# Performance work log

Hardware: AMD Instinct MI355X
Metric: run time of the kernel (lower is better)

The kernel has to match this reference:

```python
import jax, jax.numpy as jnp
import numpy as np

N_HEADS = 8
HEAD_DIM = 32
KSIZE = 3
IN_CH = 128
OUT_CH = 256


def setup_inputs() -> dict:
    key = jax.random.key(0)
    k1, k2, k3, k4 = jax.random.split(key, 4)
    x = jax.random.normal(k1, (8, IN_CH, 64, 64), dtype=jnp.float32)
    w_key = jax.random.normal(k2, (N_HEADS * HEAD_DIM, IN_CH), dtype=jnp.float32) * 0.05
    b_key = jax.random.normal(k3, (N_HEADS * HEAD_DIM,), dtype=jnp.float32) * 0.05
    # memory init in torch: uniform in [-1, 1)
    memory = jax.random.uniform(k4, (N_HEADS, HEAD_DIM * KSIZE * KSIZE, OUT_CH // N_HEADS),
                                dtype=jnp.float32) * 2.0 - 1.0
    return {"x": x, "w_key": w_key, "b_key": b_key, "memory": memory}


def _unfold(z, k):
    # z: [b, C, Hp, Wp] padded; returns [b, C*k*k, H*W] with torch.unfold layout
    b, C, Hp, Wp = z.shape
    H, W = Hp - k + 1, Wp - k + 1
    patches = [z[:, :, i:i + H, j:j + W] for i in range(k) for j in range(k)]
    # stack -> [b, C, k*k, H, W]; channel-major like torch unfold (C outer, kh*k+kw inner)
    p = jnp.stack(patches, axis=2)
    return p.reshape(b, C * k * k, H * W)


def reference(x, w_key, b_key, memory):
    b, c_in, H, W = x.shape
    k = KSIZE
    m = N_HEADS
    # 1x1 conv (to_mem_key)
    key_map = jnp.einsum('oi,bihw->bohw', w_key, x) + b_key[None, :, None, None]
    # ZeroPad2d((k//2, k%2, k//2, k%2)) = (left, right, top, bottom)
    pl, pr = k // 2, k % 2
    padded = jnp.pad(key_map, ((0, 0), (0, 0), (pl, pr), (pl, pr)))
    unf = _unfold(padded, k)                      # [b, C*k*k, L], C = m*head_dim
    ckk = unf.shape[1]
    L = unf.shape[2]
    c = ckk // m
    # rearrange 'b (c m) l -> b m c l' (m is the FAST factor, per einops pattern)
    attn = unf.reshape(b, c, m, L).transpose(0, 2, 1, 3)   # [b, m, c, L]
    attn = jax.nn.softmax(attn, axis=2)
    out = jnp.einsum('nki,bnkl->bnil', memory, attn)       # [b, m, head_out, L]
    # rearrange 'b m c (h w) -> b (m c) h w'
    return out.reshape(b, m * out.shape[2], H, W)
```

## Files before the change

kernel.cpp:

```cpp
#include <hip/hip_runtime.h>

#define B_   8
#define CIN  128
#define CKEY 256
#define NH   8
#define HOUT 32
#define CPH  288
#define HW   4096

#define XSTR   136
#define ESTR   264
#define EROW   (66 * ESTR)
#define E2_BYTES   (3 * EROW * 2)
#define XBUF_BYTES (64 * XSTR * 2)
#define SMEM_BYTES (E2_BYTES + 2 * XBUF_BYTES)

typedef __attribute__((ext_vector_type(8))) short bf16x8;
typedef __attribute__((ext_vector_type(4))) float f32x4;

__device__ __forceinline__ unsigned short f2bf(float f) {
  unsigned u = __builtin_bit_cast(unsigned, f);
  u += 0x7FFFu + ((u >> 16) & 1u);
  return (unsigned short)(u >> 16);
}

__global__ __launch_bounds__(256) void wfragP_prep(
    const float* __restrict__ wk, unsigned short* __restrict__ wfragP)
{
  const int idx  = blockIdx.x * 256 + threadIdx.x;
  const int lane = idx & 63, fi = idx >> 6;
  const int ks = fi & 3, sh = (fi >> 2) & 1, cm = fi >> 3;
  const int li = lane & 15, q = lane >> 4;
  const int och = cm + 8 * (sh * 16 + li);
  const int ic0 = ks * 32 + q * 8;
  unsigned short* dst = wfragP + (size_t)idx * 8;
#pragma unroll
  for (int j = 0; j < 8; ++j) dst[j] = f2bf(wk[och * CIN + ic0 + j]);
}

__global__ __launch_bounds__(256) void mfragP_prep(
    const float* __restrict__ mem, unsigned short* __restrict__ mfragP)
{
  const int idx  = blockIdx.x * 256 + threadIdx.x;
  const int lane = idx & 63, fi = idx >> 6;
  const int ib = fi & 1, pm = fi >> 1;
  const int p = pm % 9, m = pm / 9;
  const int li = lane & 15, q = lane >> 4;
  const int i  = ib * 16 + li;
  unsigned short* dst = mfragP + (size_t)idx * 8;
#pragma unroll
  for (int j = 0; j < 8; ++j) {
    const int s = q * 8 + j;
    const int c = ((m - p + 8) & 7) + 8 * s;
    const int t = (9 * c + p) >> 3;
    dst[j] = f2bf(mem[(m * CPH + t) * HOUT + i]);
  }
}

__global__ __launch_bounds__(512, 2) void fused_kernel(
    const float* __restrict__ x, const unsigned short* __restrict__ wfragP,
    const unsigned short* __restrict__ mfragP, const float* __restrict__ bk,
    float* __restrict__ out)
{
  extern __shared__ char smem[];
  unsigned short* e2  = (unsigned short*)smem;
  unsigned short* xb0 = (unsigned short*)(smem + E2_BYTES);
  unsigned short* xb1 = xb0 + 64 * XSTR;
  float* tileb = (float*)(smem + E2_BYTES);

  const int tid = threadIdx.x;
  const int bid = blockIdx.x;
  const int b = bid & 7, h = bid >> 3;
  const int lane = tid & 63;
  const int wv = __builtin_amdgcn_readfirstlane(tid >> 6);
  const int li = lane & 15, q = lane >> 4;

  float bias[2][4];
#pragma unroll
  for (int sh = 0; sh < 2; ++sh)
#pragma unroll
    for (int r = 0; r < 4; ++r)
      bias[sh][r] = bk[wv + 8 * (sh * 16 + 4 * q + r)];

  const int spx = tid & 63, sicg = tid >> 6;
  const int sxor = ((spx >> 3) & 7) << 3;

  auto stage_load = [&](int y, unsigned* pk) {
    const float* xr = x + (size_t)b * CIN * HW + y * 64 + spx;
#pragma unroll
    for (int r4 = 0; r4 < 4; ++r4) {
      const int ic0 = 4 * sicg + 32 * r4;
      const float v0 = xr[(size_t)(ic0 + 0) * HW];
      const float v1 = xr[(size_t)(ic0 + 1) * HW];
      const float v2 = xr[(size_t)(ic0 + 2) * HW];
      const float v3 = xr[(size_t)(ic0 + 3) * HW];
      pk[2 * r4 + 0] = (unsigned)f2bf(v0) | ((unsigned)f2bf(v1) << 16);
      pk[2 * r4 + 1] = (unsigned)f2bf(v2) | ((unsigned)f2bf(v3) << 16);
    }
  };
  auto stage_write = [&](unsigned short* xb, const unsigned* pk) {
    unsigned* xdw = (unsigned*)xb;
#pragma unroll
    for (int r4 = 0; r4 < 4; ++r4) {
      const int o = (2 * sicg + 16 * r4) ^ sxor;
      *(uint2*)(xdw + spx * 68 + o) = make_uint2(pk[2 * r4], pk[2 * r4 + 1]);
    }
  };

  auto conv_row = [&](const unsigned short* xb, int rrow) {
    f32x4 acc[2][4];
#pragma unroll
    for (int sh = 0; sh < 2; ++sh)
#pragma unroll
      for (int pt = 0; pt < 4; ++pt) {
        f32x4 cv; cv[0] = bias[sh][0]; cv[1] = bias[sh][1];
        cv[2] = bias[sh][2]; cv[3] = bias[sh][3];
        acc[sh][pt] = cv;
      }
    const unsigned* xdw = (const unsigned*)xb;
#pragma unroll
    for (int ks = 0; ks < 4; ++ks) {
      const bf16x8 a0 = *(const bf16x8*)(
          wfragP + ((size_t)(((wv * 2 + 0) * 4 + ks) * 64 + lane)) * 8);
      const bf16x8 a1 = *(const bf16x8*)(
          wfragP + ((size_t)(((wv * 2 + 1) * 4 + ks) * 64 + lane)) * 8);
#pragma unroll
      for (int pt = 0; pt < 4; ++pt) {
        const int px  = pt * 16 + li;
        const int blk = (ks * 16 + q * 4) ^ (((px >> 3) & 7) << 3);
        const bf16x8 bfr = *(const bf16x8*)(xdw + px * 68 + blk);
        acc[0][pt] = __builtin_amdgcn_mfma_f32_16x16x32_bf16(a0, bfr, acc[0][pt], 0, 0, 0);
        acc[1][pt] = __builtin_amdgcn_mfma_f32_16x16x32_bf16(a1, bfr, acc[1][pt], 0, 0, 0);
      }
    }
    unsigned short* erow = e2 + rrow * EROW;
#pragma unroll
    for (int sh = 0; sh < 2; ++sh)
#pragma unroll
      for (int pt = 0; pt < 4; ++pt) {
        const float w0 = __expf(acc[sh][pt][0]);
        const float w1 = __expf(acc[sh][pt][1]);
        const float w2 = __expf(acc[sh][pt][2]);
        const float w3 = __expf(acc[sh][pt][3]);
        const unsigned d0 = (unsigned)f2bf(w0) | ((unsigned)f2bf(w1) << 16);
        const unsigned d1 = (unsigned)f2bf(w2) | ((unsigned)f2bf(w3) << 16);
        unsigned short* dst = erow + (pt * 16 + li + 1) * ESTR
                            + wv * 32 + sh * 16 + 4 * q;
        *(uint2*)dst = make_uint2(d0, d1);
      }
    if (tid < 256) {
      const int xcol = (tid & 1) ? 65 : 0;
      ((unsigned*)(erow + xcol * ESTR))[tid >> 1] = 0x3F803F80u;
    }
  };
  auto fill_row = [&](int rrow) {
    unsigned* erow = (unsigned*)(e2 + rrow * EROW);
    for (int d = tid; d < 66 * 132; d += 512) erow[d] = 0x3F803F80u;
  };

  const bool v0r = (h - 1 >= 0), v2r = (h + 1 < 64);
  unsigned pk0[8], pk1[8], pk2[8];
  if (v0r) stage_load(h - 1, pk0);
  stage_load(h, pk1);
  if (v2r) stage_load(h + 1, pk2);
  if (v0r) stage_write(xb0, pk0);
  stage_write(xb1, pk1);
  __syncthreads();
  if (v0r) conv_row(xb0, 0); else fill_row(0);
  __syncthreads();
  if (v2r) stage_write(xb0, pk2);
  __syncthreads();
  conv_row(xb1, 1);
  if (v2r) conv_row(xb0, 2); else fill_row(2);
  __syncthreads();

  const int m = wv;
  const unsigned short* mf = mfragP + (size_t)(m * 9) * 2 * 64 * 8;
  const int4 onesi = make_int4(0x3F803F80, 0x3F803F80, 0x3F803F80, 0x3F803F80);
  const bf16x8 bones = __builtin_bit_cast(bf16x8, onesi);

  f32x4 acc[4][2], accs[4];
#pragma unroll
  for (int pb = 0; pb < 4; ++pb) {
    acc[pb][0] = {0.f, 0.f, 0.f, 0.f};
    acc[pb][1] = {0.f, 0.f, 0.f, 0.f};
    accs[pb]   = {0.f, 0.f, 0.f, 0.f};
  }

#pragma unroll
  for (int p = 0; p < 9; ++p) {
    const bf16x8 bm0 = *(const bf16x8*)(mf + ((size_t)((p * 2 + 0) * 64 + lane)) * 8);
    const bf16x8 bm1 = *(const bf16x8*)(mf + ((size_t)((p * 2 + 1) * 64 + lane)) * 8);
    const int cm   = (m - p + 8) & 7;
    const int rrow = p / 3;
    const int dxp  = p - 3 * rrow;
    const unsigned short* abase = e2 + rrow * EROW + (li + dxp) * ESTR
                                + cm * 32 + q * 8;
#pragma unroll
    for (int pb = 0; pb < 4; ++pb) {
      const bf16x8 af = *(const bf16x8*)(abase + pb * 16 * ESTR);
      acc[pb][0] = __builtin_amdgcn_mfma_f32_16x16x32_bf16(af, bm0, acc[pb][0], 0, 0, 0);
      acc[pb][1] = __builtin_amdgcn_mfma_f32_16x16x32_bf16(af, bm1, acc[pb][1], 0, 0, 0);
      accs[pb]   = __builtin_amdgcn_mfma_f32_16x16x32_bf16(af, bones, accs[pb], 0, 0, 0);
    }
  }

  float* tw = tileb + wv * (16 * 33);
  float* ob = out + ((size_t)(b * CKEY + m * HOUT)) * HW + h * 64;
#pragma unroll
  for (int pb = 0; pb < 4; ++pb) {
#pragma unroll
    for (int r = 0; r < 4; ++r) {
      const float inv = 1.0f / accs[pb][r];
      tw[(q * 4 + r) * 33 + li]      = acc[pb][0][r] * inv;
      tw[(q * 4 + r) * 33 + 16 + li] = acc[pb][1][r] * inv;
    }
#pragma unroll
    for (int s2 = 0; s2 < 8; ++s2) {
      const int i = s2 * 4 + q;
      ob[(size_t)i * HW + pb * 16 + li] = tw[li * 33 + i];
    }
  }
}

extern "C" void kernel_launch(void* const* d_in, const int* in_sizes, int n_in,
                              void* d_out, int out_size, void* d_ws, size_t ws_size,
                              hipStream_t stream) {
  const float* x   = (const float*)d_in[0];
  const float* wk  = (const float*)d_in[1];
  const float* bk  = (const float*)d_in[2];
  const float* mem = (const float*)d_in[3];

  unsigned short* wfragP = (unsigned short*)d_ws;
  unsigned short* mfragP = (unsigned short*)((char*)d_ws + 65536);

  static int attr_set = 0;
  if (!attr_set) {
    hipFuncSetAttribute((const void*)fused_kernel,
                        hipFuncAttributeMaxDynamicSharedMemorySize, SMEM_BYTES);
    attr_set = 1;
  }

  wfragP_prep<<<dim3(16), dim3(256), 0, stream>>>(wk, wfragP);
  mfragP_prep<<<dim3(36), dim3(256), 0, stream>>>(mem, mfragP);
  fused_kernel<<<dim3(512), dim3(512), SMEM_BYTES, stream>>>(
      x, wfragP, mfragP, bk, (float*)d_out);
}
```

Before: 101.6 us.

## Compute two output rows per block to reuse halo key rows, merge prep kernels

Each block now produces two output rows, so it computes four conv/exp rows instead of three per output row. This cuts the redundant 1x1 conv recomputation of halo rows from 3x to 2x. The two weight-prep kernels are merged into one launch, and bf16 packing uses the HIP intrinsic. In exchange the grid halves to 256 blocks, shared memory grows to four exp rows with a single x buffer, and the row convs are serialized with extra barriers, which may reduce occupancy and latency hiding.

```diff
diff --git a/kernel.cpp b/kernel.cpp
--- a/kernel.cpp
+++ b/kernel.cpp
@@ -1,4 +1,5 @@
 #include <hip/hip_runtime.h>
+#include <hip/hip_bf16.h>
 
 #define B_   8
 #define CIN  128
@@ -8,52 +9,57 @@
 #define CPH  288
 #define HW   4096
 
-#define XSTR   136
 #define ESTR   264
 #define EROW   (66 * ESTR)
-#define E2_BYTES   (3 * EROW * 2)
-#define XBUF_BYTES (64 * XSTR * 2)
-#define SMEM_BYTES (E2_BYTES + 2 * XBUF_BYTES)
+#define E2_BYTES   (4 * EROW * 2)
+#define XBUF_BYTES (64 * 136 * 2)
+#define SMEM_BYTES (E2_BYTES + XBUF_BYTES)
 
 typedef __attribute__((ext_vector_type(8))) short bf16x8;
 typedef __attribute__((ext_vector_type(4))) float f32x4;
 
+__device__ __forceinline__ unsigned bfpack2(float a, float b) {
+  __hip_bfloat162 h = __float22bfloat162_rn(float2{a, b});
+  unsigned r;
+  __builtin_memcpy(&r, &h, 4);
+  return r;
+}
 __device__ __forceinline__ unsigned short f2bf(float f) {
   unsigned u = __builtin_bit_cast(unsigned, f);
   u += 0x7FFFu + ((u >> 16) & 1u);
   return (unsigned short)(u >> 16);
 }
 
-__global__ __launch_bounds__(256) void wfragP_prep(
-    const float* __restrict__ wk, unsigned short* __restrict__ wfragP)
+__global__ __launch_bounds__(256) void prep_kernel(
+    const float* __restrict__ wk, const float* __restrict__ mem,
+    unsigned short* __restrict__ wfragP, unsigned short* __restrict__ mfragP)
 {
-  const int idx  = blockIdx.x * 256 + threadIdx.x;
-  const int lane = idx & 63, fi = idx >> 6;
-  const int ks = fi & 3, sh = (fi >> 2) & 1, cm = fi >> 3;
-  const int li = lane & 15, q = lane >> 4;
-  const int och = cm + 8 * (sh * 16 + li);
-  const int ic0 = ks * 32 + q * 8;
-  unsigned short* dst = wfragP + (size_t)idx * 8;
-#pragma unroll
-  for (int j = 0; j < 8; ++j) dst[j] = f2bf(wk[och * CIN + ic0 + j]);
-}
-
-__global__ __launch_bounds__(256) void mfragP_prep(
-    const float* __restrict__ mem, unsigned short* __restrict__ mfragP)
-{
-  const int idx  = blockIdx.x * 256 + threadIdx.x;
-  const int lane = idx & 63, fi = idx >> 6;
-  const int ib = fi & 1, pm = fi >> 1;
-  const int p = pm % 9, m = pm / 9;
-  const int li = lane & 15, q = lane >> 4;
-  const int i  = ib * 16 + li;
-  unsigned short* dst = mfragP + (size_t)idx * 8;
-#pragma unroll
-  for (int j = 0; j < 8; ++j) {
-    const int s = q * 8 + j;
-    const int c = ((m - p + 8) & 7) + 8 * s;
-    const int t = (9 * c + p) >> 3;
-    dst[j] = f2bf(mem[(m * CPH + t) * HOUT + i]);
+  const int gb = blockIdx.x;
+  if (gb < 16) {
+    const int idx  = gb * 256 + threadIdx.x;
+    const int lane = idx & 63, fi = idx >> 6;
+    const int ks = fi & 3, sh = (fi >> 2) & 1, cm = fi >> 3;
+    const int li = lane & 15, q = lane >> 4;
+    const int och = cm + 8 * (sh * 16 + li);
+    const int ic0 = ks * 32 + q * 8;
+    unsigned short* dst = wfragP + (size_t)idx * 8;
+#pragma unroll
+    for (int j = 0; j < 8; ++j) dst[j] = f2bf(wk[och * CIN + ic0 + j]);
+  } else {
+    const int idx  = (gb - 16) * 256 + threadIdx.x;
+    const int lane = idx & 63, fi = idx >> 6;
+    const int ib = fi & 1, pm = fi >> 1;
+    const int p = pm % 9, m = pm / 9;
+    const int li = lane & 15, q = lane >> 4;
+    const int i  = ib * 16 + li;
+    unsigned short* dst = mfragP + (size_t)idx * 8;
+#pragma unroll
+    for (int j = 0; j < 8; ++j) {
+      const int s = q * 8 + j;
+      const int c = ((m - p + 8) & 7) + 8 * s;
+      const int t = (9 * c + p) >> 3;
+      dst[j] = f2bf(mem[(m * CPH + t) * HOUT + i]);
+    }
   }
 }
 
@@ -63,14 +69,14 @@
     float* __restrict__ out)
 {
   extern __shared__ char smem[];
-  unsigned short* e2  = (unsigned short*)smem;
-  unsigned short* xb0 = (unsigned short*)(smem + E2_BYTES);
-  unsigned short* xb1 = xb0 + 64 * XSTR;
-  float* tileb = (float*)(smem + E2_BYTES);
+  unsigned short* e2 = (unsigned short*)smem;
+  unsigned*       xdw = (unsigned*)(smem + E2_BYTES);
+  float*          tileb = (float*)(smem + E2_BYTES);
 
   const int tid = threadIdx.x;
   const int bid = blockIdx.x;
-  const int b = bid & 7, h = bid >> 3;
+  const int b  = bid & 7;
+  const int h0 = (bid >> 3) * 2;
   const int lane = tid & 63;
   const int wv = __builtin_amdgcn_readfirstlane(tid >> 6);
   const int li = lane & 15, q = lane >> 4;
@@ -85,7 +91,12 @@
   const int spx = tid & 63, sicg = tid >> 6;
   const int sxor = ((spx >> 3) & 7) << 3;
 
-  auto stage_load = [&](int y, unsigned* pk) {
+  const bool valid[4] = {h0 - 1 >= 0, true, true, h0 + 2 < 64};
+  unsigned pk[4][8];
+#pragma unroll
+  for (int r = 0; r < 4; ++r) {
+    if (!valid[r]) continue;
+    const int y = h0 - 1 + r;
     const float* xr = x + (size_t)b * CIN * HW + y * 64 + spx;
 #pragma unroll
     for (int r4 = 0; r4 < 4; ++r4) {
@@ -94,131 +105,121 @@
       const float v1 = xr[(size_t)(ic0 + 1) * HW];
       const float v2 = xr[(size_t)(ic0 + 2) * HW];
       const float v3 = xr[(size_t)(ic0 + 3) * HW];
-      pk[2 * r4 + 0] = (unsigned)f2bf(v0) | ((unsigned)f2bf(v1) << 16);
-      pk[2 * r4 + 1] = (unsigned)f2bf(v2) | ((unsigned)f2bf(v3) << 16);
-    }
-  };
-  auto stage_write = [&](unsigned short* xb, const unsigned* pk) {
-    unsigned* xdw = (unsigned*)xb;
-#pragma unroll
-    for (int r4 = 0; r4 < 4; ++r4) {
-      const int o = (2 * sicg + 16 * r4) ^ sxor;
-      *(uint2*)(xdw + spx * 68 + o) = make_uint2(pk[2 * r4], pk[2 * r4 + 1]);
-    }
-  };
-
-  auto conv_row = [&](const unsigned short* xb, int rrow) {
-    f32x4 acc[2][4];
-#pragma unroll
-    for (int sh = 0; sh < 2; ++sh)
-#pragma unroll
-      for (int pt = 0; pt < 4; ++pt) {
-        f32x4 cv; cv[0] = bias[sh][0]; cv[1] = bias[sh][1];
-        cv[2] = bias[sh][2]; cv[3] = bias[sh][3];
-        acc[sh][pt] = cv;
-      }
-    const unsigned* xdw = (const unsigned*)xb;
-#pragma unroll
-    for (int ks = 0; ks < 4; ++ks) {
-      const bf16x8 a0 = *(const bf16x8*)(
-          wfragP + ((size_t)(((wv * 2 + 0) * 4 + ks) * 64 + lane)) * 8);
-      const bf16x8 a1 = *(const bf16x8*)(
-          wfragP + ((size_t)(((wv * 2 + 1) * 4 + ks) * 64 + lane)) * 8);
-#pragma unroll
-      for (int pt = 0; pt < 4; ++pt) {
-        const int px  = pt * 16 + li;
-        const int blk = (ks * 16 + q * 4) ^ (((px >> 3) & 7) << 3);
-        const bf16x8 bfr = *(const bf16x8*)(xdw + px * 68 + blk);
-        acc[0][pt] = __builtin_amdgcn_mfma_f32_16x16x32_bf16(a0, bfr, acc[0][pt], 0, 0, 0);
-        acc[1][pt] = __builtin_amdgcn_mfma_f32_16x16x32_bf16(a1, bfr, acc[1][pt], 0, 0, 0);
-      }
-    }
-    unsigned short* erow = e2 + rrow * EROW;
-#pragma unroll
-    for (int sh = 0; sh < 2; ++sh)
-#pragma unroll
-      for (int pt = 0; pt < 4; ++pt) {
-        const float w0 = __expf(acc[sh][pt][0]);
-        const float w1 = __expf(acc[sh][pt][1]);
-        const float w2 = __expf(acc[sh][pt][2]);
-        const float w3 = __expf(acc[sh][pt][3]);
-        const unsigned d0 = (unsigned)f2bf(w0) | ((unsigned)f2bf(w1) << 16);
-        const unsigned d1 = (unsigned)f2bf(w2) | ((unsigned)f2bf(w3) << 16);
-        unsigned short* dst = erow + (pt * 16 + li + 1) * ESTR
-                            + wv * 32 + sh * 16 + 4 * q;
-        *(uint2*)dst = make_uint2(d0, d1);
-      }
-    if (tid < 256) {
-      const int xcol = (tid & 1) ? 65 : 0;
-      ((unsigned*)(erow + xcol * ESTR))[tid >> 1] = 0x3F803F80u;
-    }
-  };
-  auto fill_row = [&](int rrow) {
-    unsigned* erow = (unsigned*)(e2 + rrow * EROW);
-    for (int d = tid; d < 66 * 132; d += 512) erow[d] = 0x3F803F80u;
-  };
-
-  const bool v0r = (h - 1 >= 0), v2r = (h + 1 < 64);
-  unsigned pk0[8], pk1[8], pk2[8];
-  if (v0r) stage_load(h - 1, pk0);
-  stage_load(h, pk1);
-  if (v2r) stage_load(h + 1, pk2);
-  if (v0r) stage_write(xb0, pk0);
-  stage_write(xb1, pk1);
-  __syncthreads();
-  if (v0r) conv_row(xb0, 0); else fill_row(0);
-  __syncthreads();
-  if (v2r) stage_write(xb0, pk2);
-  __syncthreads();
-  conv_row(xb1, 1);
-  if (v2r) conv_row(xb0, 2); else fill_row(2);
-  __syncthreads();
+      pk[r][2 * r4 + 0] = bfpack2(v0, v1);
+      pk[r][2 * r4 + 1] = bfpack2(v2, v3);
+    }
+  }
+
+#pragma unroll
+  for (int r = 0; r < 4; r += 3) {
+    if (!valid[r]) {
+      unsigned* erow = (unsigned*)(e2 + r * EROW);
+      for (int d = tid; d < 66 * 132; d += 512) erow[d] = 0x3F803F80u;
+    }
+  }
+
+#pragma unroll
+  for (int rr = 0; rr < 4; ++rr) {
+    if (valid[rr]) {
+#pragma unroll
+      for (int r4 = 0; r4 < 4; ++r4) {
+        const int o = (2 * sicg + 16 * r4) ^ sxor;
+        *(uint2*)(xdw + spx * 68 + o) = make_uint2(pk[rr][2 * r4], pk[rr][2 * r4 + 1]);
+      }
+    }
+    __syncthreads();
+    if (valid[rr]) {
+      f32x4 acc[2][4];
+#pragma unroll
+      for (int sh = 0; sh < 2; ++sh)
+#pragma unroll
+        for (int pt = 0; pt < 4; ++pt) {
+          f32x4 cv; cv[0] = bias[sh][0]; cv[1] = bias[sh][1];
+          cv[2] = bias[sh][2]; cv[3] = bias[sh][3];
+          acc[sh][pt] = cv;
+        }
+#pragma unroll
+      for (int ks = 0; ks < 4; ++ks) {
+        const bf16x8 a0 = *(const bf16x8*)(
+            wfragP + ((size_t)(((wv * 2 + 0) * 4 + ks) * 64 + lane)) * 8);
+        const bf16x8 a1 = *(const bf16x8*)(
+            wfragP + ((size_t)(((wv * 2 + 1) * 4 + ks) * 64 + lane)) * 8);
+#pragma unroll
+        for (int pt = 0; pt < 4; ++pt) {
+          const int px  = pt * 16 + li;
+          const int blk = (ks * 16 + q * 4) ^ (((px >> 3) & 7) << 3);
+          const bf16x8 bfr = *(const bf16x8*)(xdw + px * 68 + blk);
+          acc[0][pt] = __builtin_amdgcn_mfma_f32_16x16x32_bf16(a0, bfr, acc[0][pt], 0, 0, 0);
+          acc[1][pt] = __builtin_amdgcn_mfma_f32_16x16x32_bf16(a1, bfr, acc[1][pt], 0, 0, 0);
+        }
+      }
+      unsigned short* erow = e2 + rr * EROW;
+#pragma unroll
+      for (int sh = 0; sh < 2; ++sh)
+#pragma unroll
+        for (int pt = 0; pt < 4; ++pt) {
+          const float w0 = __expf(acc[sh][pt][0]);
+          const float w1 = __expf(acc[sh][pt][1]);
+          const float w2 = __expf(acc[sh][pt][2]);
+          const float w3 = __expf(acc[sh][pt][3]);
+          unsigned short* dst = erow + (pt * 16 + li + 1) * ESTR
+                              + wv * 32 + sh * 16 + 4 * q;
+          *(uint2*)dst = make_uint2(bfpack2(w0, w1), bfpack2(w2, w3));
+        }
+      if (tid < 256) {
+        const int xcol = (tid & 1) ? 65 : 0;
+        ((unsigned*)(erow + xcol * ESTR))[tid >> 1] = 0x3F803F80u;
+      }
+    }
+    __syncthreads();
+  }
 
   const int m = wv;
   const unsigned short* mf = mfragP + (size_t)(m * 9) * 2 * 64 * 8;
   const int4 onesi = make_int4(0x3F803F80, 0x3F803F80, 0x3F803F80, 0x3F803F80);
   const bf16x8 bones = __builtin_bit_cast(bf16x8, onesi);
-
-  f32x4 acc[4][2], accs[4];
-#pragma unroll
-  for (int pb = 0; pb < 4; ++pb) {
-    acc[pb][0] = {0.f, 0.f, 0.f, 0.f};
-    acc[pb][1] = {0.f, 0.f, 0.f, 0.f};
-    accs[pb]   = {0.f, 0.f, 0.f, 0.f};
-  }
-
-#pragma unroll
-  for (int p = 0; p < 9; ++p) {
-    const bf16x8 bm0 = *(const bf16x8*)(mf + ((size_t)((p * 2 + 0) * 64 + lane)) * 8);
-    const bf16x8 bm1 = *(const bf16x8*)(mf + ((size_t)((p * 2 + 1) * 64 + lane)) * 8);
-    const int cm   = (m - p + 8) & 7;
-    const int rrow = p / 3;
-    const int dxp  = p - 3 * rrow;
-    const unsigned short* abase = e2 + rrow * EROW + (li + dxp) * ESTR
-                                + cm * 32 + q * 8;
+  float* tw = tileb + wv * (16 * 33);
+
+#pragma unroll
+  for (int hh = 0; hh < 2; ++hh) {
+    f32x4 acc[4][2], accs[4];
 #pragma unroll
     for (int pb = 0; pb < 4; ++pb) {
-      const bf16x8 af = *(const bf16x8*)(abase + pb * 16 * ESTR);
-      acc[pb][0] = __builtin_amdgcn_mfma_f32_16x16x32_bf16(af, bm0, acc[pb][0], 0, 0, 0);
-      acc[pb][1] = __builtin_amdgcn_mfma_f32_16x16x32_bf16(af, bm1, acc[pb][1], 0, 0, 0);
-      accs[pb]   = __builtin_amdgcn_mfma_f32_16x16x32_bf16(af, bones, accs[pb], 0, 0, 0);
-    }
-  }
-
-  float* tw = tileb + wv * (16 * 33);
-  float* ob = out + ((size_t)(b * CKEY + m * HOUT)) * HW + h * 64;
-#pragma unroll
-  for (int pb = 0; pb < 4; ++pb) {
-#pragma unroll
-    for (int r = 0; r < 4; ++r) {
-      const float inv = 1.0f / accs[pb][r];
-      tw[(q * 4 + r) * 33 + li]      = acc[pb][0][r] * inv;
-      tw[(q * 4 + r) * 33 + 16 + li] = acc[pb][1][r] * inv;
-    }
-#pragma unroll
-    for (int s2 = 0; s2 < 8; ++s2) {
-      const int i = s2 * 4 + q;
-      ob[(size_t)i * HW + pb * 16 + li] = tw[li * 33 + i];
+      acc[pb][0] = {0.f, 0.f, 0.f, 0.f};
+      acc[pb][1] = {0.f, 0.f, 0.f, 0.f};
+      accs[pb]   = {0.f, 0.f, 0.f, 0.f};
+    }
+#pragma unroll
+    for (int p = 0; p < 9; ++p) {
+      const bf16x8 bm0 = *(const bf16x8*)(mf + ((size_t)((p * 2 + 0) * 64 + lane)) * 8);
+      const bf16x8 bm1 = *(const bf16x8*)(mf + ((size_t)((p * 2 + 1) * 64 + lane)) * 8);
+      const int cm   = (m - p + 8) & 7;
+      const int rrow = hh + p / 3;
+      const int dxp  = p - 3 * (p / 3);
+      const unsigned short* abase = e2 + rrow * EROW + (li + dxp) * ESTR
+                                  + cm * 32 + q * 8;
+#pragma unroll
+      for (int pb = 0; pb < 4; ++pb) {
+        const bf16x8 af = *(const bf16x8*)(abase + pb * 16 * ESTR);
+        acc[pb][0] = __builtin_amdgcn_mfma_f32_16x16x32_bf16(af, bm0, acc[pb][0], 0, 0, 0);
+        acc[pb][1] = __builtin_amdgcn_mfma_f32_16x16x32_bf16(af, bm1, acc[pb][1], 0, 0, 0);
+        accs[pb]   = __builtin_amdgcn_mfma_f32_16x16x32_bf16(af, bones, accs[pb], 0, 0, 0);
+      }
+    }
+    float* ob = out + ((size_t)(b * CKEY + m * HOUT)) * HW + (h0 + hh) * 64;
+#pragma unroll
+    for (int pb = 0; pb < 4; ++pb) {
+#pragma unroll
+      for (int r = 0; r < 4; ++r) {
+        const float inv = 1.0f / accs[pb][r];
+        tw[(q * 4 + r) * 33 + li]      = acc[pb][0][r] * inv;
+        tw[(q * 4 + r) * 33 + 16 + li] = acc[pb][1][r] * inv;
+      }
+#pragma unroll
+      for (int s2 = 0; s2 < 8; ++s2) {
+        const int i = s2 * 4 + q;
+        ob[(size_t)i * HW + pb * 16 + li] = tw[li * 33 + i];
+      }
     }
   }
 }
@@ -234,15 +235,10 @@
   unsigned short* wfragP = (unsigned short*)d_ws;
   unsigned short* mfragP = (unsigned short*)((char*)d_ws + 65536);
 
-  static int attr_set = 0;
-  if (!attr_set) {
-    hipFuncSetAttribute((const void*)fused_kernel,
-                        hipFuncAttributeMaxDynamicSharedMemorySize, SMEM_BYTES);
-    attr_set = 1;
-  }
-
-  wfragP_prep<<<dim3(16), dim3(256), 0, stream>>>(wk, wfragP);
-  mfragP_prep<<<dim3(36), dim3(256), 0, stream>>>(mem, mfragP);
-  fused_kernel<<<dim3(512), dim3(512), SMEM_BYTES, stream>>>(
+  (void)hipFuncSetAttribute((const void*)fused_kernel,
+                            hipFuncAttributeMaxDynamicSharedMemorySize, SMEM_BYTES);
+
+  prep_kernel<<<dim3(52), dim3(256), 0, stream>>>(wk, mem, wfragP, mfragP);
+  fused_kernel<<<dim3(256), dim3(512), SMEM_BYTES, stream>>>(
       x, wfragP, mfragP, bk, (float*)d_out);
 }
```

Measured after the change: 94.69 us. 6.8% less time.
